# Optimization experiments

Hardware: AMD Instinct MI355X
Metric: run time of the kernel (lower is better)

The kernel has to match this reference:

```python
import jax, jax.numpy as jnp
import numpy as np

EOS_IDX = 2
B, S, T = 512, 64, 32
V, E, H, DENC, L = 128, 256, 512, 1024, 2


def setup_inputs() -> dict:
    key = jax.random.key(0)
    ks = jax.random.split(key, 24)
    s = 0.02
    inp = {
        "encoder_out": jax.random.normal(ks[0], (B, S, DENC), jnp.float32),
        "h0": jax.random.normal(ks[1], (L, B, H), jnp.float32),
        "c0": jax.random.normal(ks[2], (L, B, H), jnp.float32),
        "targets": jax.random.randint(ks[3], (B, T), 0, V),
        "mask": jax.random.randint(ks[4], (B, S), 0, 2).astype(jnp.int32),
        # parameters
        "emb": jax.random.normal(ks[5], (V, E), jnp.float32) * s,
        "W_enc": jax.random.normal(ks[6], (H, DENC), jnp.float32) * s,
        "W_dec": jax.random.normal(ks[7], (H, H), jnp.float32) * s,
        "v": jax.random.normal(ks[8], (H,), jnp.float32) * s,
        "W_ih0": jax.random.normal(ks[9], (4 * H, E + DENC), jnp.float32) * s,
        "W_hh0": jax.random.normal(ks[10], (4 * H, H), jnp.float32) * s,
        "b_ih0": jax.random.normal(ks[11], (4 * H,), jnp.float32) * s,
        "b_hh0": jax.random.normal(ks[12], (4 * H,), jnp.float32) * s,
        "W_ih1": jax.random.normal(ks[13], (4 * H, H), jnp.float32) * s,
        "W_hh1": jax.random.normal(ks[14], (4 * H, H), jnp.float32) * s,
        "b_ih1": jax.random.normal(ks[15], (4 * H,), jnp.float32) * s,
        "b_hh1": jax.random.normal(ks[16], (4 * H,), jnp.float32) * s,
        "W_out": jax.random.normal(ks[17], (V, H + DENC + E), jnp.float32) * s,
        "b_out": jax.random.normal(ks[18], (V,), jnp.float32) * s,
    }
    # guarantee at least one valid source position per row
    inp["mask"] = inp["mask"].at[:, 0].set(1)
    return inp


def _lstm_cell(x, h, c, W_ih, W_hh, b_ih, b_hh):
    gates = x @ W_ih.T + b_ih + h @ W_hh.T + b_hh  # (B, 4H)
    i, f, g, o = jnp.split(gates, 4, axis=-1)      # torch gate order i,f,g,o
    c_new = jax.nn.sigmoid(f) * c + jax.nn.sigmoid(i) * jnp.tanh(g)
    h_new = jax.nn.sigmoid(o) * jnp.tanh(c_new)
    return h_new, c_new


def reference(encoder_out, h0, c0, targets, mask,
              emb, W_enc, W_dec, v,
              W_ih0, W_hh0, b_ih0, b_hh0,
              W_ih1, W_hh1, b_ih1, b_hh1,
              W_out, b_out):
    # teacher_forcing_ratio = 1.0: input tokens are [EOS, targets[:, :-1]]
    tokens = jnp.concatenate(
        [jnp.full((targets.shape[0], 1), EOS_IDX, dtype=targets.dtype),
         targets[:, :-1]], axis=1)                       # (B, T)
    embedded = emb[tokens]                               # (B, T, E)
    enc_proj = jnp.einsum('bsd,hd->bsh', encoder_out, W_enc)  # precompute W_enc(encoder_out)
    mask_b = mask > 0                                    # (B, S)

    def step(carry, x_emb):                              # x_emb: (B, E)
        h, c = carry                                     # each (L, B, H)
        h_top = h[-1]                                    # (B, H)
        dec_proj = h_top @ W_dec.T                       # (B, H)
        energy = jnp.tanh(dec_proj[:, None, :] + enc_proj)   # (B, S, H)
        score = jnp.einsum('bsh,h->bs', energy, v)       # (B, S)
        score = jnp.where(mask_b, score, -jnp.inf)
        weights = jax.nn.softmax(score, axis=-1)         # (B, S)
        context = jnp.einsum('bs,bsd->bd', weights, encoder_out)  # (B, DENC)
        x = jnp.concatenate([x_emb, context], axis=-1)   # (B, E+DENC)
        h0n, c0n = _lstm_cell(x, h[0], c[0], W_ih0, W_hh0, b_ih0, b_hh0)
        h1n, c1n = _lstm_cell(h0n, h[1], c[1], W_ih1, W_hh1, b_ih1, b_hh1)
        pred = jnp.concatenate([h1n, context, x_emb], axis=-1) @ W_out.T + b_out  # (B, V)
        return (jnp.stack([h0n, h1n]), jnp.stack([c0n, c1n])), pred

    (_, _), preds = jax.lax.scan(step, (h0, c0), jnp.swapaxes(embedded, 0, 1))
    return jnp.swapaxes(preds, 0, 1)                     # (B, T, V)
```

## Files before the change

### kernel.cpp

```cpp
#include <hip/hip_runtime.h>
#include <math.h>

#define BB 512
#define SS 64
#define TT 32
#define VV 128
#define EE 256
#define HH 512
#define DENC 1024
#define BH (BB*HH)
#define XW0 1792
#define XW1 1024
#define PW  1792
#define G4H 2048

typedef __attribute__((ext_vector_type(8))) short bf16x8;
typedef __attribute__((ext_vector_type(4))) short bf16x4;
typedef __attribute__((ext_vector_type(4))) float f32x4;

__device__ __forceinline__ float sigf(float x){ return 1.f/(1.f+expf(-x)); }
__device__ __forceinline__ float bf2f(short s){
  return __uint_as_float(((unsigned)(unsigned short)s) << 16);
}
__device__ __forceinline__ short f2bf(float f){
  unsigned u = __float_as_uint(f);
  return (short)((u + 0x7FFF + ((u>>16)&1)) >> 16);
}
__device__ __forceinline__ float tanh_fast(float x){
  x = fminf(fmaxf(x, -15.f), 15.f);
  float e = __expf(2.f*x);
  return (e - 1.f) / (e + 1.f);
}

__device__ __forceinline__ void zacc(f32x4 a[2][2]){
  #pragma unroll
  for (int i = 0; i < 2; ++i)
    #pragma unroll
    for (int j = 0; j < 2; ++j) a[i][j] = {0.f,0.f,0.f,0.f};
}

template<int BM, int BN>
struct GemmPipe {
  static constexpr int LA = 72;
  static __device__ __forceinline__ void run(short* Asb, short* Bsb,
      const short* __restrict__ A, const short* __restrict__ Bt,
      int lda, int ldb, int kBase, int nIter,
      int rowBase, int colBase, int tid, f32x4 acc[BM/32][BN/32])
  {
    constexpr int FI = BM/32, FJ = BN/32, ACH = BM/32, BCH = BN/32;
    const int lane = tid & 63, wave = tid >> 6;
    const int ml = lane & 15, kq = lane >> 4;
    const int wm = (wave >> 1)*(BM/2), wn = (wave & 1)*(BN/2);
    const int arow = (tid*ACH) >> 3, acol = ((tid*ACH) & 7)*8;
    const int brow = (tid*BCH) >> 3, bcol = ((tid*BCH) & 7)*8;
    const short* Ap = A + (size_t)(rowBase+arow)*lda + kBase + acol;
    const short* Bp = Bt + (size_t)(colBase+brow)*ldb + kBase + bcol;
    bf16x8 ar[ACH], br[BCH];
    #pragma unroll
    for (int c = 0; c < ACH; ++c) ar[c] = *(const bf16x8*)(Ap + c*8);
    #pragma unroll
    for (int c = 0; c < BCH; ++c) br[c] = *(const bf16x8*)(Bp + c*8);
    for (int i = 0; i < nIter; ++i) {
      short* Ab = Asb + (i&1)*(BM*LA);
      short* Bb = Bsb + (i&1)*(BN*LA);
      #pragma unroll
      for (int c = 0; c < ACH; ++c) *(bf16x8*)&Ab[arow*LA + acol + c*8] = ar[c];
      #pragma unroll
      for (int c = 0; c < BCH; ++c) *(bf16x8*)&Bb[brow*LA + bcol + c*8] = br[c];
      __syncthreads();
      if (i+1 < nIter) {
        const short* An = Ap + (size_t)(i+1)*64;
        const short* Bn = Bp + (size_t)(i+1)*64;
        #pragma unroll
        for (int c = 0; c < ACH; ++c) ar[c] = *(const bf16x8*)(An + c*8);
        #pragma unroll
        for (int c = 0; c < BCH; ++c) br[c] = *(const bf16x8*)(Bn + c*8);
      }
      #pragma unroll
      for (int kh = 0; kh < 2; ++kh) {
        bf16x8 af[FI], bfv[FJ];
        #pragma unroll
        for (int ii = 0; ii < FI; ++ii)
          af[ii] = *(const bf16x8*)&Ab[(wm + ii*16 + ml)*LA + kh*32 + kq*8];
        #pragma unroll
        for (int jj = 0; jj < FJ; ++jj)
          bfv[jj] = *(const bf16x8*)&Bb[(wn + jj*16 + ml)*LA + kh*32 + kq*8];
        #pragma unroll
        for (int ii = 0; ii < FI; ++ii)
          #pragma unroll
          for (int jj = 0; jj < FJ; ++jj)
            acc[ii][jj] = __builtin_amdgcn_mfma_f32_16x16x32_bf16(af[ii], bfv[jj], acc[ii][jj], 0,0,0);
      }
    }
    __syncthreads();
  }
};


__device__ __forceinline__ void attn_role(int aid, int tid, char* smem, int t,
    const short* __restrict__ enc_proj, const short* __restrict__ enc_out,
    const float* __restrict__ vvec, const int* __restrict__ mask,
    const int* __restrict__ targets, const short* __restrict__ embb,
    const short* __restrict__ hb, const short* __restrict__ wdecT,
    short* __restrict__ xcat0, short* __restrict__ predcat)
{
  const int b0 = aid*2;
  float* hbf = (float*)smem;
  float* dps = (float*)(smem + 4096);
  float* vvf = (float*)(smem + 12288);
  float* sc  = (float*)(smem + 14336);
  float* wt  = (float*)(smem + 14848);
  {
    bf16x4 h4 = *(const bf16x4*)&hb[(size_t)b0*HH + tid*4];
    #pragma unroll
    for (int j = 0; j < 4; ++j) hbf[tid*4 + j] = bf2f(h4[j]);
    vvf[tid] = vvec[tid];
    vvf[256 + tid] = vvec[256 + tid];
  }
  __syncthreads();
  {
    int unit = tid & 127, ksel = tid >> 7;
    int bb = unit >> 6, h8 = unit & 63;
    const short* wp = wdecT + (size_t)(ksel*256)*HH + h8*8;
    const float* hrow = hbf + bb*HH + ksel*256;
    float a[8] = {0.f,0.f,0.f,0.f,0.f,0.f,0.f,0.f};
    for (int k = 0; k < 256; ++k) {
      bf16x8 w8 = *(const bf16x8*)(wp + (size_t)k*HH);
      float x = hrow[k];
      #pragma unroll
      for (int j = 0; j < 8; ++j) a[j] += x * bf2f(w8[j]);
    }
    float* d = dps + (ksel*2 + bb)*HH + h8*8;
    #pragma unroll
    for (int j = 0; j < 8; ++j) d[j] = a[j];
  }
  __syncthreads();
  {
    int bb = tid >> 7, h0_ = (tid & 127)*4;
    f32x4 s0 = *(f32x4*)&dps[bb*HH + h0_];
    f32x4 s1 = *(f32x4*)&dps[(2 + bb)*HH + h0_];
    *(f32x4*)&dps[bb*HH + h0_] = s0 + s1;
  }
  __syncthreads();
  {
    int u = tid >> 1, khalf = tid & 1;
    int bb = u >> 6, s = u & 63;
    const short* ep = enc_proj + ((size_t)(b0+bb)*SS + s)*HH + khalf*256;
    const float* dpp = dps + bb*HH + khalf*256;
    const float* vp  = vvf + khalf*256;
    float accv = 0.f;
    for (int hc = 0; hc < 32; ++hc) {
      bf16x8 e8 = *(const bf16x8*)(ep + hc*8);
      f32x4 d0 = *(const f32x4*)(dpp + hc*8);
      f32x4 d1 = *(const f32x4*)(dpp + hc*8 + 4);
      f32x4 v0 = *(const f32x4*)(vp + hc*8);
      f32x4 v1 = *(const f32x4*)(vp + hc*8 + 4);
      #pragma unroll
      for (int j = 0; j < 4; ++j) accv += v0[j]*tanh_fast(d0[j] + bf2f(e8[j]));
      #pragma unroll
      for (int j = 0; j < 4; ++j) accv += v1[j]*tanh_fast(d1[j] + bf2f(e8[4+j]));
    }
    accv += __shfl_xor(accv, 1, 64);
    if (khalf == 0) sc[bb*64 + s] = accv;
  }
  __syncthreads();
  if (tid < 128) {
    int bb = tid >> 6, s = tid & 63;
    int valid = mask[(b0+bb)*SS + s];
    float x = valid ? sc[bb*64 + s] : -INFINITY;
    float mx = x;
    #pragma unroll
    for (int off = 32; off; off >>= 1) mx = fmaxf(mx, __shfl_xor(mx, off, 64));
    float e = valid ? __expf(x - mx) : 0.f;
    float sum = e;
    #pragma unroll
    for (int off = 32; off; off >>= 1) sum += __shfl_xor(sum, off, 64);
    wt[bb*64 + s] = e / sum;
  }
  __syncthreads();
  {
    int bb = tid >> 7, d0 = (tid & 127)*8;
    const short* eob = enc_out + (size_t)(b0+bb)*SS*DENC + d0;
    float ca[8] = {0.f,0.f,0.f,0.f,0.f,0.f,0.f,0.f};
    for (int s = 0; s < SS; ++s) {
      float w = wt[bb*64 + s];
      bf16x8 e8 = *(const bf16x8*)(eob + (size_t)s*DENC);
      #pragma unroll
      for (int j = 0; j < 8; ++j) ca[j] += w * bf2f(e8[j]);
    }
    bf16x8 cb8;
    #pragma unroll
    for (int j = 0; j < 8; ++j) cb8[j] = f2bf(ca[j]);
    int b_ = b0 + bb;
    *(bf16x8*)&xcat0[(size_t)b_*XW0 + EE + d0] = cb8;
    *(bf16x8*)&predcat[(size_t)b_*PW + HH + d0] = cb8;
  }
  #pragma unroll
  for (int bb = 0; bb < 2; ++bb) {
    int b_ = b0 + bb;
    int tok = (t == 0) ? 2 : targets[b_*TT + t - 1];
    predcat[(size_t)b_*PW + HH + DENC + tid] = embb[tok*EE + tid];
  }
}

__device__ __forceinline__ void out_role(int idx, int tid, char* smem,
    const short* __restrict__ predprev, const short* __restrict__ wout,
    const float* __restrict__ b_out, float* __restrict__ out, int t)
{
  short* As = (short*)smem;
  short* Bs = (short*)(smem + 18432);
  const int rowBase = (idx >> 1)*64, colBase = (idx & 1)*64;
  f32x4 acc[2][2];
  zacc(acc);
  GemmPipe<64,64>::run(As, Bs, predprev, wout, PW, PW, 0, PW/64, rowBase, colBase, tid, acc);
  const int lane = tid & 63, wave = tid >> 6, ml = lane & 15, kq = lane >> 4;
  const int wm = (wave >> 1)*32, wn = (wave & 1)*32;
  #pragma unroll
  for (int ii = 0; ii < 2; ++ii)
    #pragma unroll
    for (int jj = 0; jj < 2; ++jj) {
      int n = colBase + wn + jj*16 + ml;
      float bv = b_out[n];
      #pragma unroll
      for (int r2 = 0; r2 < 4; ++r2) {
        int m = rowBase + wm + ii*16 + kq*4 + r2;
        out[(size_t)m*(TT*VV) + (size_t)(t-1)*VV + n] = acc[ii][jj][r2] + bv;
      }
    }
}

__device__ __forceinline__ void pstore(int tid, int rowBase, int colBase,
    float* __restrict__ P, f32x4 acc[2][2])
{
  const int lane = tid & 63, wave = tid >> 6, ml = lane & 15, kq = lane >> 4;
  const int wm = (wave >> 1)*32, wn = (wave & 1)*32;
  #pragma unroll
  for (int ii = 0; ii < 2; ++ii)
    #pragma unroll
    for (int jj = 0; jj < 2; ++jj)
      #pragma unroll
      for (int r2 = 0; r2 < 4; ++r2)
        P[(size_t)(rowBase + wm + ii*16 + kq*4 + r2)*G4H + colBase + wn + jj*16 + ml] = acc[ii][jj][r2];
}

__device__ __forceinline__ void gates_epi(int tid, int rowBase, int colBase,
    char* smem, f32x4 acc[2][2], const float* __restrict__ bias,
    float* __restrict__ cb,
    short* __restrict__ d1, int ld1, short* __restrict__ d2, int ld2,
    short* __restrict__ d3)
{
  const int lane = tid & 63, wave = tid >> 6, ml = lane & 15, kq = lane >> 4;
  const int wm = (wave >> 1)*32, wn = (wave & 1)*32;
  float* Ct = (float*)smem;
  float bj0 = bias[colBase + wn + ml];
  float bj1 = bias[colBase + wn + 16 + ml];
  #pragma unroll
  for (int ii = 0; ii < 2; ++ii)
    #pragma unroll
    for (int jj = 0; jj < 2; ++jj)
      #pragma unroll
      for (int r2 = 0; r2 < 4; ++r2)
        Ct[(wm + ii*16 + kq*4 + r2)*68 + wn + jj*16 + ml] = acc[ii][jj][r2] + (jj ? bj1 : bj0);
  __syncthreads();
  #pragma unroll
  for (int kk = 0; kk < 4; ++kk) {
    int cidx = tid + kk*256;
    int m = cidx >> 4, hl = cidx & 15;
    float4 gv = *(float4*)&Ct[m*68 + hl*4];
    int b_ = rowBase + m, h_ = (colBase >> 2) + hl;
    float cp = cb[b_*HH + h_];
    float cn = sigf(gv.y)*cp + sigf(gv.x)*tanhf(gv.z);
    float hn = sigf(gv.w)*tanhf(cn);
    cb[b_*HH + h_] = cn;
    short hb16 = f2bf(hn);
    d1[(size_t)b_*ld1 + h_] = hb16;
    d2[(size_t)b_*ld2 + h_] = hb16;
    if (d3) d3[(size_t)b_*HH + h_] = hb16;
  }
}

__device__ __forceinline__ void emb_prewrite(int rowBase, int tid,
    short* __restrict__ xc0n, const int* __restrict__ targets,
    const short* __restrict__ embb, int t)
{
  int b_ = rowBase + (tid >> 2);
  int tok = targets[b_*TT + t];
  const short* src = embb + tok*EE + (tid & 3)*64;
  short* dst = xc0n + (size_t)b_*XW0 + (tid & 3)*64;
  #pragma unroll
  for (int j = 0; j < 8; ++j)
    *(bf16x8*)(dst + j*8) = *(const bf16x8*)(src + j*8);
}


__global__ __launch_bounds__(256)
void attn_pg0(const short* __restrict__ enc_proj, const short* __restrict__ enc_out,
              const float* __restrict__ vvec, const int* __restrict__ mask,
              const int* __restrict__ targets, const short* __restrict__ embb,
              const short* __restrict__ hb, const short* __restrict__ wdecT,
              short* __restrict__ xcat0, short* __restrict__ predcat,
              const short* __restrict__ wcat0, float* __restrict__ P0,
              const short* __restrict__ predprev, const short* __restrict__ wout,
              const float* __restrict__ b_out, float* __restrict__ out, int t)
{
  __shared__ __align__(16) char smem[36864];
  const int tid = threadIdx.x, bid = blockIdx.x;
  if (bid < 256) {
    attn_role(bid, tid, smem, t, enc_proj, enc_out, vvec, mask, targets,
              embb, hb, wdecT, xcat0, predcat);
  } else if (bid < 512) {
    short* As = (short*)smem;
    short* Bs = (short*)(smem + 18432);
    int idx = bid - 256;
    int rowBase = (idx >> 5)*64, colBase = (idx & 31)*64;
    f32x4 acc[2][2];
    zacc(acc);
    GemmPipe<64,64>::run(As, Bs, xcat0, wcat0, XW0, XW0, 0,    4, rowBase, colBase, tid, acc);
    GemmPipe<64,64>::run(As, Bs, xcat0, wcat0, XW0, XW0, 1280, 8, rowBase, colBase, tid, acc);
    pstore(tid, rowBase, colBase, P0, acc);
  } else {
    if (t >= 1) out_role(bid - 512, tid, smem, predprev, wout, b_out, out, t);
  }
}

__global__ __launch_bounds__(256)
void gates0_fin(const short* __restrict__ A, const short* __restrict__ W,
                const float* __restrict__ bias, const float* __restrict__ P0,
                float* __restrict__ cb,
                short* __restrict__ d1, short* __restrict__ d2,
                short* __restrict__ xc0n, const int* __restrict__ targets,
                const short* __restrict__ embb, int t)
{
  __shared__ __align__(16) char smem[36864];
  const int tid = threadIdx.x, bid = blockIdx.x;
  if (bid >= 256) {
    if (t + 1 < TT) emb_prewrite((bid - 256)*64, tid, xc0n, targets, embb, t);
    return;
  }
  short* As = (short*)smem;
  short* Bs = (short*)(smem + 18432);
  const int rowBase = (bid >> 5)*64, colBase = (bid & 31)*64;
  const int lane = tid & 63, wave = tid >> 6, ml = lane & 15, kq = lane >> 4;
  const int wm = (wave >> 1)*32, wn = (wave & 1)*32;
  f32x4 acc[2][2];
  const float* Pp = P0 + (size_t)rowBase*G4H + colBase;
  #pragma unroll
  for (int ii = 0; ii < 2; ++ii)
    #pragma unroll
    for (int jj = 0; jj < 2; ++jj)
      #pragma unroll
      for (int r2 = 0; r2 < 4; ++r2)
        acc[ii][jj][r2] = Pp[(wm + ii*16 + kq*4 + r2)*G4H + wn + jj*16 + ml];
  GemmPipe<64,64>::run(As, Bs, A, W, XW0, XW0, 256, 16, rowBase, colBase, tid, acc);
  gates_epi(tid, rowBase, colBase, smem, acc, bias, cb, d1, XW1, d2, XW0, (short*)nullptr);
}

__global__ __launch_bounds__(256)
void gates1_full(const short* __restrict__ A, const short* __restrict__ W,
                 const float* __restrict__ bias, float* __restrict__ cb,
                 short* __restrict__ d1, short* __restrict__ d2, short* __restrict__ d3)
{
  __shared__ __align__(16) char smem[36864];
  const int tid = threadIdx.x, bid = blockIdx.x;
  short* As = (short*)smem;
  short* Bs = (short*)(smem + 18432);
  const int rowBase = (bid >> 5)*64, colBase = (bid & 31)*64;
  f32x4 acc[2][2];
  zacc(acc);
  GemmPipe<64,64>::run(As, Bs, A, W, XW1, XW1, 0, 16, rowBase, colBase, tid, acc);
  gates_epi(tid, rowBase, colBase, smem, acc, bias, cb, d1, XW1, d2, PW, d3);
}

__global__ __launch_bounds__(256)
void out_fin(const short* __restrict__ predprev, const short* __restrict__ wout,
             const float* __restrict__ b_out, float* __restrict__ out)
{
  __shared__ __align__(16) char smem[36864];
  out_role(blockIdx.x, threadIdx.x, smem, predprev, wout, b_out, out, TT);
}

__global__ __launch_bounds__(256)
void enc_gemm(short* __restrict__ C, const short* __restrict__ A, const short* __restrict__ Bt,
              int K, int ldc)
{
  __shared__ __align__(16) char smem[55296];
  short* As = (short*)smem;
  short* Bs = (short*)(smem + 18432);
  const int tid = threadIdx.x;
  const int rowBase = blockIdx.y*64, colBase = blockIdx.x*128;
  f32x4 acc[2][4];
  #pragma unroll
  for (int i = 0; i < 2; ++i)
    #pragma unroll
    for (int j = 0; j < 4; ++j) acc[i][j] = {0.f,0.f,0.f,0.f};
  GemmPipe<64,128>::run(As, Bs, A, Bt, K, K, 0, K >> 6, rowBase, colBase, tid, acc);
  const int lane = tid & 63, wave = tid >> 6, ml = lane & 15, kq = lane >> 4;
  const int wm = (wave >> 1)*32, wn = (wave & 1)*64;
  #pragma unroll
  for (int ii = 0; ii < 2; ++ii)
    #pragma unroll
    for (int jj = 0; jj < 4; ++jj) {
      int n = colBase + wn + jj*16 + ml;
      #pragma unroll
      for (int r2 = 0; r2 < 4; ++r2) {
        int m = rowBase + wm + ii*16 + kq*4 + r2;
        C[(size_t)m*ldc + n] = f2bf(acc[ii][jj][r2]);
      }
    }
}

__global__ __launch_bounds__(256)
void build_wcat_bf(short* __restrict__ wcat0, short* __restrict__ wcat1,
                   const float* __restrict__ wih0, const float* __restrict__ whh0,
                   const float* __restrict__ wih1, const float* __restrict__ whh1)
{
  int idx = blockIdx.x*256 + threadIdx.x;
  const int N0 = G4H*XW0;
  if (idx < N0) {
    int n = idx / XW0, k = idx % XW0;
    int row = (n & 3)*HH + (n >> 2);
    float v = (k < EE+DENC) ? wih0[(size_t)row*(EE+DENC) + k] : whh0[(size_t)row*HH + (k - (EE+DENC))];
    wcat0[idx] = f2bf(v);
  } else {
    int j = idx - N0;
    int n = j / XW1, k = j % XW1;
    int row = (n & 3)*HH + (n >> 2);
    float v = (k < HH) ? wih1[(size_t)row*HH + k] : whh1[(size_t)row*HH + (k - HH)];
    wcat1[j] = f2bf(v);
  }
}

__global__ __launch_bounds__(256)
void cvt_encout(short* __restrict__ dst, const float* __restrict__ src)
{
  size_t i8 = ((size_t)blockIdx.x*256 + threadIdx.x)*8;
  float4 a = *(const float4*)&src[i8];
  float4 b = *(const float4*)&src[i8+4];
  bf16x8 o;
  o[0]=f2bf(a.x); o[1]=f2bf(a.y); o[2]=f2bf(a.z); o[3]=f2bf(a.w);
  o[4]=f2bf(b.x); o[5]=f2bf(b.y); o[6]=f2bf(b.z); o[7]=f2bf(b.w);
  *(bf16x8*)&dst[i8] = o;
}

__global__ __launch_bounds__(256)
void prep_misc(float* __restrict__ cbuf, short* __restrict__ xcat0a, short* __restrict__ xcat1a,
               short* __restrict__ hb, short* __restrict__ wdecT, short* __restrict__ wenc,
               short* __restrict__ wout, short* __restrict__ embb,
               float* __restrict__ bias0i, float* __restrict__ bias1i,
               const float* __restrict__ c0, const float* __restrict__ h0,
               const float* __restrict__ W_dec, const float* __restrict__ W_enc,
               const float* __restrict__ W_out, const float* __restrict__ emb,
               const float* __restrict__ b_ih0, const float* __restrict__ b_hh0,
               const float* __restrict__ b_ih1, const float* __restrict__ b_hh1)
{
  int idx = blockIdx.x*256 + threadIdx.x;
  if (idx < 524288) { cbuf[idx] = c0[idx]; return; }
  idx -= 524288;
  if (idx < 262144) {
    int b = idx >> 9, h = idx & 511;
    xcat0a[(size_t)b*XW0 + EE + DENC + h] = f2bf(h0[idx]);
    return;
  }
  idx -= 262144;
  if (idx < 262144) {
    int b = idx >> 9, h = idx & 511;
    short v = f2bf(h0[BH + idx]);
    xcat1a[(size_t)b*XW1 + HH + h] = v;
    hb[idx] = v;
    return;
  }
  idx -= 262144;
  if (idx < 262144) {
    int k = idx >> 9, n = idx & 511;
    wdecT[idx] = f2bf(W_dec[(size_t)n*HH + k]);
    return;
  }
  idx -= 262144;
  if (idx < 524288) { wenc[idx] = f2bf(W_enc[idx]); return; }
  idx -= 524288;
  if (idx < 229376) { wout[idx] = f2bf(W_out[idx]); return; }
  idx -= 229376;
  if (idx < 32768)  { embb[idx] = f2bf(emb[idx]); return; }
  idx -= 32768;
  if (idx < 2048) {
    int row = (idx & 3)*HH + (idx >> 2);
    bias0i[idx] = b_ih0[row] + b_hh0[row];
    return;
  }
  idx -= 2048;
  if (idx < 2048) {
    int row = (idx & 3)*HH + (idx >> 2);
    bias1i[idx] = b_ih1[row] + b_hh1[row];
    return;
  }
  idx -= 2048;
  {
    int b = idx >> 8, e = idx & 255;
    xcat0a[(size_t)b*XW0 + e] = f2bf(emb[2*EE + e]);
  }
}

extern "C" void kernel_launch(void* const* d_in, const int* in_sizes, int n_in,
                              void* d_out, int out_size, void* d_ws, size_t ws_size,
                              hipStream_t stream) {
  const float* enc_out = (const float*)d_in[0];
  const float* h0      = (const float*)d_in[1];
  const float* c0      = (const float*)d_in[2];
  const int*   targets = (const int*)d_in[3];
  const int*   mask    = (const int*)d_in[4];
  const float* emb     = (const float*)d_in[5];
  const float* W_enc   = (const float*)d_in[6];
  const float* W_dec   = (const float*)d_in[7];
  const float* v       = (const float*)d_in[8];
  const float* b_ih0   = (const float*)d_in[11];
  const float* b_hh0   = (const float*)d_in[12];
  const float* b_ih1   = (const float*)d_in[15];
  const float* b_hh1   = (const float*)d_in[16];
  const float* b_out   = (const float*)d_in[18];
  float* out = (float*)d_out;

  char* ws = (char*)d_ws;
  size_t o = 0;
  short* enc_out_bf = (short*)(ws + o); o += (size_t)BB*SS*DENC*2;
  short* enc_proj_bf= (short*)(ws + o); o += (size_t)BB*SS*HH*2;
  short* wcat0i     = (short*)(ws + o); o += (size_t)G4H*XW0*2;
  short* wcat1i     = (short*)(ws + o); o += (size_t)G4H*XW1*2;
  short* wdecT      = (short*)(ws + o); o += (size_t)HH*HH*2;
  short* wenc_bf    = (short*)(ws + o); o += (size_t)HH*DENC*2;
  short* wout_bf    = (short*)(ws + o); o += (size_t)VV*PW*2;
  short* emb_bf     = (short*)(ws + o); o += (size_t)VV*EE*2;
  short* xcat0a     = (short*)(ws + o); o += (size_t)BB*XW0*2;
  short* xcat0b     = (short*)(ws + o); o += (size_t)BB*XW0*2;
  short* xcat1a     = (short*)(ws + o); o += (size_t)BB*XW1*2;
  short* xcat1b     = (short*)(ws + o); o += (size_t)BB*XW1*2;
  short* predcata   = (short*)(ws + o); o += (size_t)BB*PW*2;
  short* predcatb   = (short*)(ws + o); o += (size_t)BB*PW*2;
  short* hb         = (short*)(ws + o); o += (size_t)BH*2;
  float* cbuf       = (float*)(ws + o); o += (size_t)2*BH*4;
  float* bias0i     = (float*)(ws + o); o += (size_t)G4H*4;
  float* bias1i     = (float*)(ws + o); o += (size_t)G4H*4;
  float* P0         = (float*)(ws + o); o += (size_t)BB*G4H*4;
  (void)ws_size; (void)in_sizes; (void)n_in; (void)out_size;

  cvt_encout<<<16384, 256, 0, stream>>>(enc_out_bf, enc_out);
  build_wcat_bf<<<22528, 256, 0, stream>>>(wcat0i, wcat1i,
      (const float*)d_in[9], (const float*)d_in[10], (const float*)d_in[13], (const float*)d_in[14]);
  prep_misc<<<8720, 256, 0, stream>>>(cbuf, xcat0a, xcat1a, hb, wdecT, wenc_bf, wout_bf, emb_bf,
      bias0i, bias1i, c0, h0, W_dec, W_enc, (const float*)d_in[17], emb,
      b_ih0, b_hh0, b_ih1, b_hh1);
  enc_gemm<<<dim3(HH/128, (BB*SS)/64), 256, 0, stream>>>(
      enc_proj_bf, enc_out_bf, wenc_bf, DENC, HH);

  short* xc0[2] = {xcat0a, xcat0b};
  short* xc1[2] = {xcat1a, xcat1b};
  short* pc[2]  = {predcata, predcatb};
  for (int t = 0; t < TT; ++t) {
    attn_pg0<<<528, 256, 0, stream>>>(enc_proj_bf, enc_out_bf, v, mask, targets, emb_bf,
        hb, wdecT, xc0[t&1], pc[t&1], wcat0i, P0, pc[(t+1)&1], wout_bf, b_out, out, t);
    gates0_fin<<<264, 256, 0, stream>>>(
        xc0[t&1], wcat0i, bias0i, P0, cbuf, xc1[t&1], xc0[(t+1)&1] + EE + DENC,
        xc0[(t+1)&1], targets, emb_bf, t);
    gates1_full<<<256, 256, 0, stream>>>(
        xc1[t&1], wcat1i, bias1i, cbuf + BH, xc1[(t+1)&1] + HH, pc[t&1], hb);
  }
  out_fin<<<16, 256, 0, stream>>>(pc[1], wout_bf, b_out, out);
}
```

Before: 2.797 ms.

## Precompute layer-1 recurrent gate partials and split output GEMM across K in attention kernel

The h1 half of the layer-1 gate GEMM (columns 512..1023 of xcat1, which depend only on the previous step's h1) now runs early in the attention kernel and writes fp32 partials to P1. gates1 then loads these partials and does only the remaining K half, which shortens the critical path after gates0. The output projection is split into two K-halves computed in the attention kernel, and their sum plus bias is written by extra blocks of gates0_fin. This adds fp32 partial buffer traffic and more blocks in the attention launch in exchange for less serial GEMM work per step.

```diff
diff --git a/kernel.cpp b/kernel.cpp
--- a/kernel.cpp
+++ b/kernel.cpp
@@ -294,14 +294,16 @@
 
 
 __global__ __launch_bounds__(256)
-void attn_pg0(const short* __restrict__ enc_proj, const short* __restrict__ enc_out,
-              const float* __restrict__ vvec, const int* __restrict__ mask,
-              const int* __restrict__ targets, const short* __restrict__ embb,
-              const short* __restrict__ hb, const short* __restrict__ wdecT,
-              short* __restrict__ xcat0, short* __restrict__ predcat,
-              const short* __restrict__ wcat0, float* __restrict__ P0,
-              const short* __restrict__ predprev, const short* __restrict__ wout,
-              const float* __restrict__ b_out, float* __restrict__ out, int t)
+void attn_pg01(const short* __restrict__ enc_proj, const short* __restrict__ enc_out,
+               const float* __restrict__ vvec, const int* __restrict__ mask,
+               const int* __restrict__ targets, const short* __restrict__ embb,
+               const short* __restrict__ hb, const short* __restrict__ wdecT,
+               short* __restrict__ xcat0, short* __restrict__ predcat,
+               const short* __restrict__ wcat0, float* __restrict__ P0,
+               const short* __restrict__ xcat1, const short* __restrict__ wcat1,
+               float* __restrict__ P1,
+               const short* __restrict__ predprev, const short* __restrict__ wout,
+               float* __restrict__ Pout, int t)
 {
   __shared__ __align__(16) char smem[36864];
   const int tid = threadIdx.x, bid = blockIdx.x;
@@ -318,8 +320,37 @@
     GemmPipe<64,64>::run(As, Bs, xcat0, wcat0, XW0, XW0, 0,    4, rowBase, colBase, tid, acc);
     GemmPipe<64,64>::run(As, Bs, xcat0, wcat0, XW0, XW0, 1280, 8, rowBase, colBase, tid, acc);
     pstore(tid, rowBase, colBase, P0, acc);
+  } else if (bid < 768) {
+    short* As = (short*)smem;
+    short* Bs = (short*)(smem + 18432);
+    int idx = bid - 512;
+    int rowBase = (idx >> 5)*64, colBase = (idx & 31)*64;
+    f32x4 acc[2][2];
+    zacc(acc);
+    GemmPipe<64,64>::run(As, Bs, xcat1, wcat1, XW1, XW1, 512, 8, rowBase, colBase, tid, acc);
+    pstore(tid, rowBase, colBase, P1, acc);
   } else {
-    if (t >= 1) out_role(bid - 512, tid, smem, predprev, wout, b_out, out, t);
+    if (t >= 1) {
+      short* As = (short*)smem;
+      short* Bs = (short*)(smem + 18432);
+      int idx = bid - 768;
+      int half = idx >> 4, oIdx = idx & 15;
+      int rowBase = (oIdx >> 1)*64, colBase = (oIdx & 1)*64;
+      f32x4 acc[2][2];
+      zacc(acc);
+      GemmPipe<64,64>::run(As, Bs, predprev, wout, PW, PW, half*896, 14,
+                           rowBase, colBase, tid, acc);
+      const int lane = tid & 63, wave = tid >> 6, ml = lane & 15, kq = lane >> 4;
+      const int wm = (wave >> 1)*32, wn = (wave & 1)*32;
+      float* Pt = Pout + half*65536;
+      #pragma unroll
+      for (int ii = 0; ii < 2; ++ii)
+        #pragma unroll
+        for (int jj = 0; jj < 2; ++jj)
+          #pragma unroll
+          for (int r2 = 0; r2 < 4; ++r2)
+            Pt[(rowBase + wm + ii*16 + kq*4 + r2)*VV + colBase + wn + jj*16 + ml] = acc[ii][jj][r2];
+    }
   }
 }
 
@@ -329,10 +360,28 @@
                 float* __restrict__ cb,
                 short* __restrict__ d1, short* __restrict__ d2,
                 short* __restrict__ xc0n, const int* __restrict__ targets,
-                const short* __restrict__ embb, int t)
+                const short* __restrict__ embb,
+                const float* __restrict__ Pout, const float* __restrict__ b_out,
+                float* __restrict__ out, int t)
 {
   __shared__ __align__(16) char smem[36864];
   const int tid = threadIdx.x, bid = blockIdx.x;
+  if (bid >= 264) {
+    if (t >= 1) {
+      int base = (bid - 264)*8192 + tid*32;
+      #pragma unroll
+      for (int j = 0; j < 8; ++j) {
+        int i = base + j*4;
+        f32x4 a = *(const f32x4*)&Pout[i];
+        f32x4 b = *(const f32x4*)&Pout[65536 + i];
+        int m = i >> 7, n = i & 127;
+        f32x4 bo = *(const f32x4*)&b_out[n];
+        f32x4 r = a + b + bo;
+        *(f32x4*)&out[(size_t)m*(TT*VV) + (size_t)(t-1)*VV + n] = r;
+      }
+    }
+    return;
+  }
   if (bid >= 256) {
     if (t + 1 < TT) emb_prewrite((bid - 256)*64, tid, xc0n, targets, embb, t);
     return;
@@ -356,18 +405,28 @@
 }
 
 __global__ __launch_bounds__(256)
-void gates1_full(const short* __restrict__ A, const short* __restrict__ W,
-                 const float* __restrict__ bias, float* __restrict__ cb,
-                 short* __restrict__ d1, short* __restrict__ d2, short* __restrict__ d3)
+void gates1_fin(const short* __restrict__ A, const short* __restrict__ W,
+                const float* __restrict__ bias, const float* __restrict__ P1,
+                float* __restrict__ cb,
+                short* __restrict__ d1, short* __restrict__ d2, short* __restrict__ d3)
 {
   __shared__ __align__(16) char smem[36864];
   const int tid = threadIdx.x, bid = blockIdx.x;
   short* As = (short*)smem;
   short* Bs = (short*)(smem + 18432);
   const int rowBase = (bid >> 5)*64, colBase = (bid & 31)*64;
+  const int lane = tid & 63, wave = tid >> 6, ml = lane & 15, kq = lane >> 4;
+  const int wm = (wave >> 1)*32, wn = (wave & 1)*32;
   f32x4 acc[2][2];
-  zacc(acc);
-  GemmPipe<64,64>::run(As, Bs, A, W, XW1, XW1, 0, 16, rowBase, colBase, tid, acc);
+  const float* Pp = P1 + (size_t)rowBase*G4H + colBase;
+  #pragma unroll
+  for (int ii = 0; ii < 2; ++ii)
+    #pragma unroll
+    for (int jj = 0; jj < 2; ++jj)
+      #pragma unroll
+      for (int r2 = 0; r2 < 4; ++r2)
+        acc[ii][jj][r2] = Pp[(wm + ii*16 + kq*4 + r2)*G4H + wn + jj*16 + ml];
+  GemmPipe<64,64>::run(As, Bs, A, W, XW1, XW1, 0, 8, rowBase, colBase, tid, acc);
   gates_epi(tid, rowBase, colBase, smem, acc, bias, cb, d1, XW1, d2, PW, d3);
 }
 
@@ -540,6 +599,8 @@
   float* bias0i     = (float*)(ws + o); o += (size_t)G4H*4;
   float* bias1i     = (float*)(ws + o); o += (size_t)G4H*4;
   float* P0         = (float*)(ws + o); o += (size_t)BB*G4H*4;
+  float* P1         = (float*)(ws + o); o += (size_t)BB*G4H*4;
+  float* Pout       = (float*)(ws + o); o += (size_t)2*BB*VV*4;
   (void)ws_size; (void)in_sizes; (void)n_in; (void)out_size;
 
   cvt_encout<<<16384, 256, 0, stream>>>(enc_out_bf, enc_out);
@@ -555,13 +616,14 @@
   short* xc1[2] = {xcat1a, xcat1b};
   short* pc[2]  = {predcata, predcatb};
   for (int t = 0; t < TT; ++t) {
-    attn_pg0<<<528, 256, 0, stream>>>(enc_proj_bf, enc_out_bf, v, mask, targets, emb_bf,
-        hb, wdecT, xc0[t&1], pc[t&1], wcat0i, P0, pc[(t+1)&1], wout_bf, b_out, out, t);
-    gates0_fin<<<264, 256, 0, stream>>>(
+    attn_pg01<<<800, 256, 0, stream>>>(enc_proj_bf, enc_out_bf, v, mask, targets, emb_bf,
+        hb, wdecT, xc0[t&1], pc[t&1], wcat0i, P0, xc1[t&1], wcat1i, P1,
+        pc[(t+1)&1], wout_bf, Pout, t);
+    gates0_fin<<<272, 256, 0, stream>>>(
         xc0[t&1], wcat0i, bias0i, P0, cbuf, xc1[t&1], xc0[(t+1)&1] + EE + DENC,
-        xc0[(t+1)&1], targets, emb_bf, t);
-    gates1_full<<<256, 256, 0, stream>>>(
-        xc1[t&1], wcat1i, bias1i, cbuf + BH, xc1[(t+1)&1] + HH, pc[t&1], hb);
+        xc0[(t+1)&1], targets, emb_bf, Pout, b_out, out, t);
+    gates1_fin<<<256, 256, 0, stream>>>(
+        xc1[t&1], wcat1i, bias1i, P1, cbuf + BH, xc1[(t+1)&1] + HH, pc[t&1], hb);
   }
   out_fin<<<16, 256, 0, stream>>>(pc[1], wout_bf, b_out, out);
 }
```

New measurement: 2.674 ms. 4.4% less time.
